# Optimization experiments

Measured on AMD Instinct MI355X. Metric: run time of the kernel, lower is better.

The kernel has to match this reference:

```python
import jax, jax.numpy as jnp
import numpy as np

TAU = 0.5
EPS = 1e-8  # torch CosineSimilarity eps


def _normalize(v):
    # matches torch cosine sim: divide by max(||v||, eps)
    n = jnp.linalg.norm(v, axis=-1, keepdims=True)
    return v / jnp.maximum(n, EPS)


def setup_inputs() -> dict:
    key = jax.random.key(0)
    k1, k2 = jax.random.split(key)
    N, D = 4096, 256
    x = jax.random.normal(k1, (N, D), dtype=jnp.float32)
    y = jax.random.normal(k2, (N, D), dtype=jnp.float32)
    return {"x": x, "y": y}


def reference(x, y):
    n = x.shape[0]
    xn = _normalize(x)
    yn = _normalize(y)
    inv_tau = 1.0 / TAU
    sim_xx = (xn @ xn.T) * inv_tau  # [n, n]
    sim_yy = (yn @ yn.T) * inv_tau
    sim_xy = (xn @ yn.T) * inv_tau
    neg_inf = jnp.float32(-jnp.inf)
    diag = jnp.arange(n)
    sim_xx = sim_xx.at[diag, diag].set(neg_inf)
    sim_yy = sim_yy.at[diag, diag].set(neg_inf)
    scores1 = jnp.concatenate([sim_xy, sim_xx], axis=-1)          # [n, 2n]
    scores2 = jnp.concatenate([sim_yy, sim_xy.T], axis=-1)        # [n, 2n]
    scores = jnp.concatenate([scores1, scores2], axis=-2)          # [2n, 2n]
    targets = jnp.arange(2 * n)
    logp = jax.nn.log_softmax(scores, axis=-1)
    loss = -jnp.mean(logp[jnp.arange(2 * n), targets])
    return loss
```

## Files before the change

kernel.cpp:

```cpp
#include <hip/hip_runtime.h>
#include <hip/hip_bf16.h>


#define NROWS 8192
#define DDIM  256
#define BM    128
#define BN    64
#define COLSPLIT 8
#define COLS_PER (NROWS / COLSPLIT)

typedef __attribute__((ext_vector_type(8))) __bf16 bf16x8_t;
typedef __attribute__((ext_vector_type(4))) float  f32x4_t;

typedef __attribute__((address_space(1))) const void* as1_cvp;
typedef __attribute__((address_space(3))) void*       as3_vp;

#if __has_builtin(__builtin_amdgcn_exp2f)
#define EXP2F __builtin_amdgcn_exp2f
#else
#define EXP2F exp2f
#endif

#define TWO_LOG2E 2.8853900817779268f

__global__ __launch_bounds__(256) void normalize_diag_kernel(
    const float* __restrict__ x, const float* __restrict__ y,
    __hip_bfloat16* __restrict__ zb, float* __restrict__ rowdiag) {
  const int w = threadIdx.x >> 6, lane = threadIdx.x & 63;
  const int i = blockIdx.x * 4 + w;
  const float4 xv = ((const float4*)(x + (size_t)i * DDIM))[lane];
  const float4 yv = ((const float4*)(y + (size_t)i * DDIM))[lane];
  float ssx = xv.x * xv.x + xv.y * xv.y + xv.z * xv.z + xv.w * xv.w;
  float ssy = yv.x * yv.x + yv.y * yv.y + yv.z * yv.z + yv.w * yv.w;
  float sxy = xv.x * yv.x + xv.y * yv.y + xv.z * yv.z + xv.w * yv.w;
  #pragma unroll
  for (int off = 32; off > 0; off >>= 1) {
    ssx += __shfl_xor(ssx, off, 64);
    ssy += __shfl_xor(ssy, off, 64);
    sxy += __shfl_xor(sxy, off, 64);
  }
  const float sclx = 1.0f / fmaxf(sqrtf(ssx), 1e-8f);
  const float scly = 1.0f / fmaxf(sqrtf(ssy), 1e-8f);
  __hip_bfloat16 px[4], py[4];
  px[0] = __float2bfloat16(xv.x * sclx); px[1] = __float2bfloat16(xv.y * sclx);
  px[2] = __float2bfloat16(xv.z * sclx); px[3] = __float2bfloat16(xv.w * sclx);
  py[0] = __float2bfloat16(yv.x * scly); py[1] = __float2bfloat16(yv.y * scly);
  py[2] = __float2bfloat16(yv.z * scly); py[3] = __float2bfloat16(yv.w * scly);
  *(short4*)(zb + (size_t)i * DDIM + lane * 4)            = *(short4*)px;
  *(short4*)(zb + (size_t)(i + 4096) * DDIM + lane * 4)   = *(short4*)py;
  if (lane == 0) rowdiag[i] = 2.0f * sxy * sclx * scly;
}

__global__ __launch_bounds__(512) void gram_lse_kernel(
    const __hip_bfloat16* __restrict__ zbh, float* __restrict__ rowsum) {
  __shared__ short smem[BN * DDIM];

  const short* zs = (const short*)zbh;
  const int tid  = threadIdx.x;
  const int w    = tid >> 6;
  const int lane = tid & 63;
  const int lhi  = lane >> 4;
  const int llo  = lane & 15;
  const int i0 = (blockIdx.x >> 3) * BM;
  const int c0 = (blockIdx.x & 7) * COLS_PER;

  const int arow = i0 + w * 16 + llo;
  bf16x8_t afrag[8];
  #pragma unroll
  for (int ks = 0; ks < 8; ++ks) {
    afrag[ks] = *(const bf16x8_t*)(zs + (size_t)arow * DDIM + ks * 32 + lhi * 8);
  }

  float racc[4] = {0.f, 0.f, 0.f, 0.f};

  for (int ct = 0; ct < COLS_PER / BN; ++ct) {
    const int cb = c0 + ct * BN;
    #pragma unroll
    for (int it = 0; it < 4; ++it) {
      const int o    = w * 4096 + it * 1024 + lane * 16;
      const int cr   = o >> 9;
      const int slot = (o >> 4) & 31;
      const size_t src_byte = (size_t)(cb + cr) * 512 + (size_t)((slot ^ (cr & 31)) << 4);
      __builtin_amdgcn_global_load_lds(
          (as1_cvp)((const char*)zs + src_byte),
          (as3_vp)((char*)smem + w * 4096 + it * 1024),
          16, 0, 0);
    }
    asm volatile("s_waitcnt vmcnt(0)" ::: "memory");
    __syncthreads();

    #pragma unroll
    for (int nt = 0; nt < 4; ++nt) {
      const int cr = nt * 16 + llo;
      f32x4_t acc = {0.f, 0.f, 0.f, 0.f};
      #pragma unroll
      for (int ks = 0; ks < 8; ++ks) {
        const int kg = ks * 4 + lhi;
        const bf16x8_t bfrag = *(const bf16x8_t*)(
            (const char*)smem + cr * 512 + ((kg ^ (cr & 31)) << 4));
        acc = __builtin_amdgcn_mfma_f32_16x16x32_bf16(afrag[ks], bfrag, acc, 0, 0, 0);
      }
      const int gc = cb + cr;
      #pragma unroll
      for (int j = 0; j < 4; ++j) {
        const int gr = i0 + w * 16 + lhi * 4 + j;
        racc[j] += (gr != gc) ? EXP2F(acc[j] * TWO_LOG2E) : 0.f;
      }
    }
    __syncthreads();
  }

  #pragma unroll
  for (int j = 0; j < 4; ++j) {
    float v = racc[j];
    v += __shfl_xor(v, 1, 16);
    v += __shfl_xor(v, 2, 16);
    v += __shfl_xor(v, 4, 16);
    v += __shfl_xor(v, 8, 16);
    if (llo == 0) {
      const int gr = i0 + w * 16 + lhi * 4 + j;
      atomicAdd(&rowsum[gr], v);
    }
  }
}

__global__ __launch_bounds__(256) void finalize_kernel(
    const float* __restrict__ rowsum, const float* __restrict__ rowdiag,
    float* __restrict__ out) {
  const int t = threadIdx.x;
  float s = 0.f;
  for (int r = t; r < NROWS; r += 256) s += __logf(rowsum[r]);
  for (int i = t; i < 4096; i += 256) s -= 2.0f * rowdiag[i];
  #pragma unroll
  for (int off = 32; off > 0; off >>= 1) s += __shfl_xor(s, off, 64);
  __shared__ float wsum[4];
  const int w = t >> 6, lane = t & 63;
  if (lane == 0) wsum[w] = s;
  __syncthreads();
  if (t == 0) out[0] = (wsum[0] + wsum[1] + wsum[2] + wsum[3]) / (float)NROWS;
}

extern "C" void kernel_launch(void* const* d_in, const int* in_sizes, int n_in,
                              void* d_out, int out_size, void* d_ws, size_t ws_size,
                              hipStream_t stream) {
  const float* x = (const float*)d_in[0];
  const float* y = (const float*)d_in[1];
  float* out = (float*)d_out;

  char* ws = (char*)d_ws;
  __hip_bfloat16* zb = (__hip_bfloat16*)ws;
  float* rowsum  = (float*)(ws + (size_t)NROWS * DDIM * 2);
  float* rowdiag = rowsum + NROWS;

  normalize_diag_kernel<<<1024, 256, 0, stream>>>(x, y, zb, rowdiag);
  hipMemsetAsync(rowsum, 0, NROWS * sizeof(float), stream);
  gram_lse_kernel<<<512, 512, 0, stream>>>(zb, rowsum);
  finalize_kernel<<<1, 256, 0, stream>>>(rowsum, rowdiag, out);
}
```

Measured before the change: 65.62 us.

## Double-buffer LDS tiles, fold exp scale into A, specialize diagonal blocks, fuse memset

The gram kernel now double-buffers the LDS column tile, issuing the async global-to-LDS loads for the next tile before computing the current one. The 2*log2(e) scale is folded into the A fragments, which removes a multiply per exp but adds extra bf16 rounding error. The diagonal mask is applied only in blocks that contain diagonal entries. The separate memset is replaced by zeroing inside the normalize kernel, and the finalize kernel uses vectorized float4 loads. Doubling LDS to 64KB per block may reduce occupancy.

```diff
diff --git a/kernel.cpp b/kernel.cpp
--- a/kernel.cpp
+++ b/kernel.cpp
@@ -8,6 +8,7 @@
 #define BN    64
 #define COLSPLIT 8
 #define COLS_PER (NROWS / COLSPLIT)
+#define NT (COLS_PER / BN)
 
 typedef __attribute__((ext_vector_type(8))) __bf16 bf16x8_t;
 typedef __attribute__((ext_vector_type(4))) float  f32x4_t;
@@ -25,7 +26,11 @@
 
 __global__ __launch_bounds__(256) void normalize_diag_kernel(
     const float* __restrict__ x, const float* __restrict__ y,
-    __hip_bfloat16* __restrict__ zb, float* __restrict__ rowdiag) {
+    __hip_bfloat16* __restrict__ zb, float* __restrict__ rowdiag,
+    float* __restrict__ rowsum) {
+  const int g = blockIdx.x * 256 + threadIdx.x;
+  if (g < NROWS) rowsum[g] = 0.f;
+
   const int w = threadIdx.x >> 6, lane = threadIdx.x & 63;
   const int i = blockIdx.x * 4 + w;
   const float4 xv = ((const float4*)(x + (size_t)i * DDIM))[lane];
@@ -53,9 +58,10 @@
 
 __global__ __launch_bounds__(512) void gram_lse_kernel(
     const __hip_bfloat16* __restrict__ zbh, float* __restrict__ rowsum) {
-  __shared__ short smem[BN * DDIM];
+  __shared__ short smem[2][BN * DDIM];
 
   const short* zs = (const short*)zbh;
+  const char* zbytes = (const char*)zs;
   const int tid  = threadIdx.x;
   const int w    = tid >> 6;
   const int lane = tid & 63;
@@ -63,31 +69,51 @@
   const int llo  = lane & 15;
   const int i0 = (blockIdx.x >> 3) * BM;
   const int c0 = (blockIdx.x & 7) * COLS_PER;
+  const bool has_diag = ((blockIdx.x >> 6) == (blockIdx.x & 7));
 
   const int arow = i0 + w * 16 + llo;
+  const float TBF = __bfloat162float(__float2bfloat16(TWO_LOG2E));
   bf16x8_t afrag[8];
   #pragma unroll
   for (int ks = 0; ks < 8; ++ks) {
     afrag[ks] = *(const bf16x8_t*)(zs + (size_t)arow * DDIM + ks * 32 + lhi * 8);
+    #pragma unroll
+    for (int e = 0; e < 8; ++e) {
+      afrag[ks][e] = (__bf16)((float)afrag[ks][e] * TBF);
+    }
   }
 
+  size_t soff[4]; int loff[4];
+  #pragma unroll
+  for (int it = 0; it < 4; ++it) {
+    const int o    = w * 4096 + it * 1024 + lane * 16;
+    const int cr   = o >> 9;
+    const int slot = (o >> 4) & 31;
+    soff[it] = (size_t)cr * 512 + (size_t)((slot ^ (cr & 31)) << 4);
+    loff[it] = w * 4096 + it * 1024;
+  }
+
+#define STAGE(buf, ct_) do {                                                  \
+    const size_t cbase = (size_t)(c0 + (ct_) * BN) * 512;                     \
+    _Pragma("unroll")                                                         \
+    for (int it = 0; it < 4; ++it) {                                          \
+      __builtin_amdgcn_global_load_lds(                                       \
+          (as1_cvp)(zbytes + cbase + soff[it]),                               \
+          (as3_vp)((char*)smem[buf] + loff[it]), 16, 0, 0);                   \
+    }                                                                         \
+  } while (0)
+
   float racc[4] = {0.f, 0.f, 0.f, 0.f};
+  const int gr_base = i0 + w * 16 + lhi * 4;
 
-  for (int ct = 0; ct < COLS_PER / BN; ++ct) {
+  STAGE(0, 0);
+  asm volatile("s_waitcnt vmcnt(0)" ::: "memory");
+  __syncthreads();
+  int cur = 0;
+
+  for (int ct = 0; ct < NT; ++ct) {
+    if (ct + 1 < NT) STAGE(cur ^ 1, ct + 1);
     const int cb = c0 + ct * BN;
-    #pragma unroll
-    for (int it = 0; it < 4; ++it) {
-      const int o    = w * 4096 + it * 1024 + lane * 16;
-      const int cr   = o >> 9;
-      const int slot = (o >> 4) & 31;
-      const size_t src_byte = (size_t)(cb + cr) * 512 + (size_t)((slot ^ (cr & 31)) << 4);
-      __builtin_amdgcn_global_load_lds(
-          (as1_cvp)((const char*)zs + src_byte),
-          (as3_vp)((char*)smem + w * 4096 + it * 1024),
-          16, 0, 0);
-    }
-    asm volatile("s_waitcnt vmcnt(0)" ::: "memory");
-    __syncthreads();
 
     #pragma unroll
     for (int nt = 0; nt < 4; ++nt) {
@@ -97,18 +123,25 @@
       for (int ks = 0; ks < 8; ++ks) {
         const int kg = ks * 4 + lhi;
         const bf16x8_t bfrag = *(const bf16x8_t*)(
-            (const char*)smem + cr * 512 + ((kg ^ (cr & 31)) << 4));
+            (const char*)smem[cur] + cr * 512 + ((kg ^ (cr & 31)) << 4));
         acc = __builtin_amdgcn_mfma_f32_16x16x32_bf16(afrag[ks], bfrag, acc, 0, 0, 0);
       }
-      const int gc = cb + cr;
-      #pragma unroll
-      for (int j = 0; j < 4; ++j) {
-        const int gr = i0 + w * 16 + lhi * 4 + j;
-        racc[j] += (gr != gc) ? EXP2F(acc[j] * TWO_LOG2E) : 0.f;
+      if (has_diag) {
+        const int gc = cb + cr;
+        #pragma unroll
+        for (int j = 0; j < 4; ++j)
+          racc[j] += ((gr_base + j) != gc) ? EXP2F(acc[j]) : 0.f;
+      } else {
+        #pragma unroll
+        for (int j = 0; j < 4; ++j)
+          racc[j] += EXP2F(acc[j]);
       }
     }
+    asm volatile("s_waitcnt vmcnt(0)" ::: "memory");
     __syncthreads();
+    cur ^= 1;
   }
+#undef STAGE
 
   #pragma unroll
   for (int j = 0; j < 4; ++j) {
@@ -117,10 +150,7 @@
     v += __shfl_xor(v, 2, 16);
     v += __shfl_xor(v, 4, 16);
     v += __shfl_xor(v, 8, 16);
-    if (llo == 0) {
-      const int gr = i0 + w * 16 + lhi * 4 + j;
-      atomicAdd(&rowsum[gr], v);
-    }
+    if (llo == 0) atomicAdd(&rowsum[gr_base + j], v);
   }
 }
 
@@ -129,8 +159,14 @@
     float* __restrict__ out) {
   const int t = threadIdx.x;
   float s = 0.f;
-  for (int r = t; r < NROWS; r += 256) s += __logf(rowsum[r]);
-  for (int i = t; i < 4096; i += 256) s -= 2.0f * rowdiag[i];
+  for (int r4 = t; r4 < NROWS / 4; r4 += 256) {
+    const float4 v = ((const float4*)rowsum)[r4];
+    s += __logf(v.x) + __logf(v.y) + __logf(v.z) + __logf(v.w);
+  }
+  for (int i4 = t; i4 < 4096 / 4; i4 += 256) {
+    const float4 d = ((const float4*)rowdiag)[i4];
+    s -= 2.0f * (d.x + d.y + d.z + d.w);
+  }
   #pragma unroll
   for (int off = 32; off > 0; off >>= 1) s += __shfl_xor(s, off, 64);
   __shared__ float wsum[4];
@@ -152,8 +188,7 @@
   float* rowsum  = (float*)(ws + (size_t)NROWS * DDIM * 2);
   float* rowdiag = rowsum + NROWS;
 
-  normalize_diag_kernel<<<1024, 256, 0, stream>>>(x, y, zb, rowdiag);
-  hipMemsetAsync(rowsum, 0, NROWS * sizeof(float), stream);
+  normalize_diag_kernel<<<1024, 256, 0, stream>>>(x, y, zb, rowdiag, rowsum);
   gram_lse_kernel<<<512, 512, 0, stream>>>(zb, rowsum);
   finalize_kernel<<<1, 256, 0, stream>>>(rowsum, rowdiag, out);
 }
```

Measured after the change: 55.35 us. 15.7% less time.
